# Kernel tuning notes

Measured on AMD Instinct MI355X. Metric: run time of the kernel, lower is better.

## Reference

```python
import jax, jax.numpy as jnp
import numpy as np
from functools import partial

INPUT_DIM = 256
HIDDEN = 512
NUM_LAYERS = 2

def _linp(key, fan_in, shape):
    # torch nn.Linear/Conv default init: U(-1/sqrt(fan_in), 1/sqrt(fan_in))
    bound = 1.0 / np.sqrt(fan_in)
    return jax.random.uniform(key, shape, jnp.float32, -bound, bound)

def setup_inputs() -> dict:
    key = jax.random.key(0)
    ks = iter(jax.random.split(key, 64))
    d = {}
    d["x"] = jax.random.normal(next(ks), (32, 16, 1, 64, 64), jnp.float32)
    # encoder convs (OIHW)
    d["conv1_w"] = _linp(next(ks), 1 * 9, (16, 1, 3, 3));   d["conv1_b"] = _linp(next(ks), 1 * 9, (16,))
    d["conv2_w"] = _linp(next(ks), 16 * 9, (32, 16, 3, 3)); d["conv2_b"] = _linp(next(ks), 16 * 9, (32,))
    d["conv3_w"] = _linp(next(ks), 32 * 9, (INPUT_DIM, 32, 3, 3)); d["conv3_b"] = _linp(next(ks), 32 * 9, (INPUT_DIM,))
    # LSTM cells: per layer 4 gate linears (forget, input, cell, output), in = input+hidden
    for j in range(NUM_LAYERS):
        fan = (INPUT_DIM if j == 0 else HIDDEN) + HIDDEN
        for g in ("f", "i", "g", "o"):
            d[f"W{g}{j}"] = _linp(next(ks), fan, (fan, HIDDEN))
            d[f"b{g}{j}"] = _linp(next(ks), fan, (HIDDEN,))
    # classifier
    d["cw1"] = _linp(next(ks), HIDDEN, (HIDDEN, 128)); d["cb1"] = _linp(next(ks), HIDDEN, (128,))
    d["cw2"] = _linp(next(ks), 128, (128, 64));        d["cb2"] = _linp(next(ks), 128, (64,))
    d["cw3"] = _linp(next(ks), 64, (64, 6));           d["cb3"] = _linp(next(ks), 64, (6,))
    return d

def _conv(x, w, b):
    y = jax.lax.conv_general_dilated(x, w, (1, 1), "SAME",
                                     dimension_numbers=("NCHW", "OIHW", "NCHW"))
    return y + b[None, :, None, None]

def _maxpool2(x):
    return jax.lax.reduce_window(x, -jnp.inf, jax.lax.max,
                                 (1, 1, 2, 2), (1, 1, 2, 2), "VALID")

def reference(x, conv1_w, conv1_b, conv2_w, conv2_b, conv3_w, conv3_b,
              Wf0, bf0, Wi0, bi0, Wg0, bg0, Wo0, bo0,
              Wf1, bf1, Wi1, bi1, Wg1, bg1, Wo1, bo1,
              cw1, cb1, cw2, cb2, cw3, cb3):
    B, T, C, H, W = x.shape
    xf = x.reshape(B * T, C, H, W)
    h = _maxpool2(jax.nn.relu(_conv(xf, conv1_w, conv1_b)))
    h = _maxpool2(jax.nn.relu(_conv(h, conv2_w, conv2_b)))
    h = jax.nn.relu(_conv(h, conv3_w, conv3_b))
    emb = h.mean(axis=(2, 3)).reshape(B, T, -1)  # AdaptiveAvgPool2d((1,1)); dropout = identity (eval)

    layers = [(Wf0, bf0, Wi0, bi0, Wg0, bg0, Wo0, bo0),
              (Wf1, bf1, Wi1, bi1, Wg1, bg1, Wo1, bo1)]

    def step(carry, x_t):
        hs, cs = carry
        inp = x_t
        new_h, new_c = [], []
        for j, (Wf, bf, Wi, bi, Wg, bg, Wo, bo) in enumerate(layers):
            comb = jnp.concatenate([inp, hs[j]], axis=1)  # [B, in+H]
            f_t = jax.nn.sigmoid(comb @ Wf + bf)
            i_t = jax.nn.sigmoid(comb @ Wi + bi)
            g_t = jnp.tanh(comb @ Wg + bg)
            o_t = jax.nn.sigmoid(comb @ Wo + bo)
            c_n = f_t * cs[j] + i_t * g_t
            h_n = o_t * jnp.tanh(c_n)
            new_h.append(h_n); new_c.append(c_n)
            inp = h_n
        return (tuple(new_h), tuple(new_c)), None

    h0 = tuple(jnp.zeros((B, HIDDEN), x.dtype) for _ in range(NUM_LAYERS))
    c0 = tuple(jnp.zeros((B, HIDDEN), x.dtype) for _ in range(NUM_LAYERS))
    (hs, _), _ = jax.lax.scan(step, (h0, c0), jnp.swapaxes(emb, 0, 1))
    last = hs[-1]  # [B, HIDDEN], last timestep top-layer h (dropout = identity)

    y = jax.nn.relu(last @ cw1 + cb1)
    y = jax.nn.relu(y @ cw2 + cb2)
    return y @ cw3 + cb3  # [B, 6]
```

## Files before the change

### kernel.cpp

```cpp
#include <hip/hip_runtime.h>
#include <math.h>

__global__ void k_conv1(const float* __restrict__ x, const float* __restrict__ w,
                        const float* __restrict__ bias, float* __restrict__ out) {
  int idx = blockIdx.x * 256 + threadIdx.x;
  int ox = idx & 31, oy = (idx >> 5) & 31, oc = (idx >> 10) & 15, n = idx >> 14;
  const float* im = x + n * 4096;
  float wv[9];
#pragma unroll
  for (int i = 0; i < 9; ++i) wv[i] = w[oc * 9 + i];
  float bs = bias[oc];
  float m = 0.f;
#pragma unroll
  for (int dy = 0; dy < 2; ++dy)
#pragma unroll
    for (int dx = 0; dx < 2; ++dx) {
      int cy = oy * 2 + dy, cx = ox * 2 + dx;
      float s = bs;
#pragma unroll
      for (int ky = 0; ky < 3; ++ky) {
        int yy = cy + ky - 1;
        if (yy < 0 || yy >= 64) continue;
#pragma unroll
        for (int kx = 0; kx < 3; ++kx) {
          int xx = cx + kx - 1;
          if (xx < 0 || xx >= 64) continue;
          s += im[yy * 64 + xx] * wv[ky * 3 + kx];
        }
      }
      m = fmaxf(m, fmaxf(s, 0.f));
    }
  out[idx] = m;
}

__global__ void k_prep_w(const float* __restrict__ w2, float* __restrict__ w2t,
                         const float* __restrict__ w3, float* __restrict__ w3t) {
  int id = blockIdx.x * 256 + threadIdx.x;
  if (id < 73728) {
    int ct = id >> 8, oc = id & 255;
    int c = ct / 9, tap = ct - 9 * c;
    w3t[id] = w3[(oc * 32 + c) * 9 + tap];
  }
  if (id < 4608) {
    int ct = id >> 5, oc = id & 31;
    int c = ct / 9, tap = ct - 9 * c;
    w2t[id] = w2[(oc * 16 + c) * 9 + tap];
  }
}

__global__ __launch_bounds__(256) void k_conv2(
    const float* __restrict__ a1, const float* __restrict__ w2t,
    const float* __restrict__ bias, float* __restrict__ a2) {
  __shared__ __align__(16) float ins[8 * 1024];
  int n = blockIdx.x, ocg = blockIdx.y;
  int tid = threadIdx.x;
  int py = tid >> 4, px = tid & 15;
  int y0 = 2 * py - 1, x0 = 2 * px - 1;
  float acc[16][4] = {};
  const float* wb = w2t + ocg * 16;
  for (int ph = 0; ph < 2; ++ph) {
    __syncthreads();
    const float4* src = (const float4*)(a1 + n * 16384 + ph * 8192);
    for (int i = tid; i < 2048; i += 256) ((float4*)ins)[i] = src[i];
    __syncthreads();
    for (int c = 0; c < 8; ++c) {
      float wv[4][4];
#pragma unroll
      for (int r = 0; r < 4; ++r) {
        int y = y0 + r;
        bool vy = (y >= 0) && (y < 32);
        int yc = vy ? y : 0;
#pragma unroll
        for (int cc = 0; cc < 4; ++cc) {
          int xx = x0 + cc;
          bool vx = (xx >= 0) && (xx < 32);
          int xc = vx ? xx : 0;
          float t = ins[c * 1024 + yc * 32 + xc];
          wv[r][cc] = (vy && vx) ? t : 0.f;
        }
      }
      int ch = ph * 8 + c;
#pragma unroll
      for (int ky = 0; ky < 3; ++ky)
#pragma unroll
        for (int kx = 0; kx < 3; ++kx) {
          const float* w16 = wb + (ch * 9 + ky * 3 + kx) * 32;
#pragma unroll
          for (int i = 0; i < 4; ++i) {
            float vv = wv[(i >> 1) + ky][(i & 1) + kx];
#pragma unroll
            for (int j = 0; j < 16; ++j) acc[j][i] += vv * w16[j];
          }
        }
    }
  }
  const float* bp = bias + ocg * 16;
  float4 o[4];
#pragma unroll
  for (int j = 0; j < 16; ++j) {
    float m = fmaxf(fmaxf(acc[j][0], acc[j][1]), fmaxf(acc[j][2], acc[j][3]));
    ((float*)o)[j] = fmaxf(m + bp[j], 0.f);
  }
  float4* dst = (float4*)(a2 + (size_t)(n * 256 + tid) * 32 + ocg * 16);
#pragma unroll
  for (int q = 0; q < 4; ++q) dst[q] = o[q];
}

__global__ __launch_bounds__(256) void k_conv3(
    const float* __restrict__ a2, const float* __restrict__ w3t,
    const float* __restrict__ bias, float* __restrict__ comb0) {
  __shared__ __align__(16) float ins[324 * 12];
  float4* ins4 = (float4*)ins;
  int n = blockIdx.x, ocb = blockIdx.y;
  int tid = threadIdx.x;
  for (int i = tid; i < 972; i += 256) ins4[i] = float4{0.f, 0.f, 0.f, 0.f};
  int wvid = __builtin_amdgcn_readfirstlane(tid >> 6);
  int lane = tid & 63;
  int tr = lane >> 4, tc = lane & 15;
  float acc[4][8] = {};
  const float* wbase = w3t + ocb * 32 + wvid * 8;
  const float4* src = (const float4*)(a2 + (size_t)n * 8192);
  for (int ph = 0; ph < 4; ++ph) {
    __syncthreads();
    for (int i = tid; i < 512; i += 256) {
      int px = i >> 1, cg = i & 1;
      int p = ((px >> 4) + 1) * 18 + (px & 15) + 1;
      ins4[p * 3 + cg] = src[px * 8 + ph * 2 + cg];
    }
    __syncthreads();
    for (int cg = 0; cg < 2; ++cg) {
      float4 v[6][3];
#pragma unroll
      for (int dr = 0; dr < 6; ++dr)
#pragma unroll
        for (int dc = 0; dc < 3; ++dc)
          v[dr][dc] = ins4[((4 * tr + dr) * 18 + tc + dc) * 3 + cg];
      int chb = ph * 8 + cg * 4;
#pragma unroll
      for (int ky = 0; ky < 3; ++ky)
#pragma unroll
        for (int kx = 0; kx < 3; ++kx)
#pragma unroll
          for (int c = 0; c < 4; ++c) {
            const float* w8 = wbase + ((chb + c) * 9 + ky * 3 + kx) * 256;
#pragma unroll
            for (int i = 0; i < 4; ++i) {
              float vv = ((const float*)&v[i + ky][kx])[c];
#pragma unroll
              for (int j = 0; j < 8; ++j) acc[i][j] += vv * w8[j];
            }
          }
    }
  }
  const float* bp = bias + ocb * 32 + wvid * 8;
  int bb = n >> 4, tt = n & 15;
#pragma unroll
  for (int j = 0; j < 8; ++j) {
    float bj = bp[j];
    float s = 0.f;
#pragma unroll
    for (int i = 0; i < 4; ++i) s += fmaxf(acc[i][j] + bj, 0.f);
#pragma unroll
    for (int off = 32; off; off >>= 1) s += __shfl_down(s, off, 64);
    if (lane == 0) {
      int oc = ocb * 32 + wvid * 8 + j;
      comb0[(size_t)(tt * 768 + oc) * 32 + bb] = s * (1.f / 256.f);
    }
  }
}

__global__ void k_pack(const float* __restrict__ Wf, const float* __restrict__ Wi,
                       const float* __restrict__ Wg, const float* __restrict__ Wo,
                       float* __restrict__ p, int fan) {
  __shared__ float t[4][32][33];
  int k0 = blockIdx.x * 32, h0 = blockIdx.y * 32;
  int tx = threadIdx.x & 31, ty = threadIdx.x >> 5;
  const float* Ws[4] = {Wf, Wi, Wg, Wo};
#pragma unroll
  for (int g = 0; g < 4; ++g)
    for (int r = 0; r < 32; r += 8)
      t[g][ty + r][tx] = Ws[g][(size_t)(k0 + ty + r) * 512 + h0 + tx];
  __syncthreads();
  for (int r = 0; r < 32; r += 8) {
    int hh = ty + r;
    float4 v = {t[0][tx][hh], t[1][tx][hh], t[2][tx][hh], t[3][tx][hh]};
    ((float4*)p)[(size_t)(h0 + hh) * fan + k0 + tx] = v;
  }
}

struct Coop2Args {
  float* comb0; float* comb1;
  const float* p0; const float* p1;
  const float* b00; const float* b01; const float* b02; const float* b03;
  const float* b10; const float* b11; const float* b12; const float* b13;
  int* bar;
};

#define COOP2_LDS_BYTES (32512 * 4)

#define FMA4(acc, s, a)                                   \
  acc.x += (s) * (a).x; acc.y += (s) * (a).y;             \
  acc.z += (s) * (a).z; acc.w += (s) * (a).w;

template <bool DO0, bool DO1>
__device__ __forceinline__ void fused_step(
    int hbase, int tid, int it, const Coop2Args& A,
    const float4* __restrict__ w40, const float4* __restrict__ w41,
    float* __restrict__ gsum, float* __restrict__ pre0,
    float* __restrict__ pre1,
    float bf0, float bi0, float bg0, float bo0,
    float bf1, float bi1, float bg1, float bo1,
    float& c0reg, float& c1reg) {
  const int C0 = 768 * 32, C1 = 1024 * 32;
  const int kc = tid >> 3, bq = tid & 7;
  float4 p0f{0,0,0,0}, p0i{0,0,0,0}, p0g{0,0,0,0}, p0o{0,0,0,0};
  float4 p1f{0,0,0,0}, p1i{0,0,0,0}, p1g{0,0,0,0}, p1o{0,0,0,0};
  float4 q0f{0,0,0,0}, q0i{0,0,0,0}, q0g{0,0,0,0}, q0o{0,0,0,0};
  float4 q1f{0,0,0,0}, q1i{0,0,0,0}, q1g{0,0,0,0}, q1o{0,0,0,0};
  if constexpr (DO1) {
    const float4* a41 = (const float4*)(A.comb1 + (size_t)(it - 1) * C1)
                        + kc * 8 + bq;
#pragma unroll
    for (int kk = 0; kk < 16; ++kk) {
      float4 a = a41[kk * 512];
      float4 u = w41[kk * 64];
      float4 v = w41[1024 + kk * 64];
      FMA4(q0f, u.x, a) FMA4(q0i, u.y, a) FMA4(q0g, u.z, a) FMA4(q0o, u.w, a)
      FMA4(q1f, v.x, a) FMA4(q1i, v.y, a) FMA4(q1g, v.z, a) FMA4(q1o, v.w, a)
    }
  }
  if constexpr (DO0) {
    const float4* a40 = (const float4*)(A.comb0 + (size_t)it * C0)
                        + kc * 8 + bq;
#pragma unroll
    for (int kk = 0; kk < 12; ++kk) {
      float4 a = a40[kk * 512];
      float4 u = w40[kk * 64];
      float4 v = w40[768 + kk * 64];
      FMA4(p0f, u.x, a) FMA4(p0i, u.y, a) FMA4(p0g, u.z, a) FMA4(p0o, u.w, a)
      FMA4(p1f, v.x, a) FMA4(p1i, v.y, a) FMA4(p1g, v.z, a) FMA4(p1o, v.w, a)
    }
  }
#define GW(hsv, gv, acc) {                                            \
    float* _r = gsum + (size_t)(((hsv) * 4 + (gv)) * 32 + 4 * bq) * 67 + kc; \
    _r[0] = acc.x; _r[67] = acc.y; _r[134] = acc.z; _r[201] = acc.w; }
  __syncthreads();
  if constexpr (DO0) {
    GW(0, 0, p0f) GW(0, 1, p0i) GW(0, 2, p0g) GW(0, 3, p0o)
    GW(1, 0, p1f) GW(1, 1, p1i) GW(1, 2, p1g) GW(1, 3, p1o)
  }
  __syncthreads();
  if constexpr (DO0) {
    int row = tid & 255, half = tid >> 8;
    const float* gp = gsum + (size_t)row * 67 + half * 32;
    float s = 0.f;
#pragma unroll
    for (int q = 0; q < 32; ++q) s += gp[q];
    pre0[half * 256 + row] = s;
  }
  __syncthreads();
  if constexpr (DO1) {
    GW(0, 0, q0f) GW(0, 1, q0i) GW(0, 2, q0g) GW(0, 3, q0o)
    GW(1, 0, q1f) GW(1, 1, q1i) GW(1, 2, q1g) GW(1, 3, q1o)
  }
  __syncthreads();
  if constexpr (DO1) {
    int row = tid & 255, half = tid >> 8;
    const float* gp = gsum + (size_t)row * 67 + half * 32;
    float s = 0.f;
#pragma unroll
    for (int q = 0; q < 32; ++q) s += gp[q];
    pre1[half * 256 + row] = s;
  }
  __syncthreads();
#undef GW
  if (tid < 64) {
    int hs2 = tid >> 5, b = tid & 31, hh = hbase + hs2;
    int r = hs2 * 128 + b;
    if constexpr (DO0) {
      float fp = pre0[r] + pre0[256 + r] + bf0;
      float ip = pre0[r + 32] + pre0[256 + r + 32] + bi0;
      float gp = pre0[r + 64] + pre0[256 + r + 64] + bg0;
      float op = pre0[r + 96] + pre0[256 + r + 96] + bo0;
      float ft = 1.f / (1.f + expf(-fp));
      float it_ = 1.f / (1.f + expf(-ip));
      float gt = tanhf(gp);
      float ot = 1.f / (1.f + expf(-op));
      float cn = ft * c0reg + it_ * gt;
      c0reg = cn;
      float hn = ot * tanhf(cn);
      float* hA = A.comb0 + (size_t)(it + 1) * C0 + 256 * 32;
      float* hB = A.comb1 + (size_t)it * C1;
      __hip_atomic_store(&hA[hh * 32 + b], hn, __ATOMIC_RELAXED,
                         __HIP_MEMORY_SCOPE_AGENT);
      __hip_atomic_store(&hB[hh * 32 + b], hn, __ATOMIC_RELAXED,
                         __HIP_MEMORY_SCOPE_AGENT);
    }
    if constexpr (DO1) {
      float fp = pre1[r] + pre1[256 + r] + bf1;
      float ip = pre1[r + 32] + pre1[256 + r + 32] + bi1;
      float gp = pre1[r + 64] + pre1[256 + r + 64] + bg1;
      float op = pre1[r + 96] + pre1[256 + r + 96] + bo1;
      float ft = 1.f / (1.f + expf(-fp));
      float it_ = 1.f / (1.f + expf(-ip));
      float gt = tanhf(gp);
      float ot = 1.f / (1.f + expf(-op));
      float cn = ft * c1reg + it_ * gt;
      c1reg = cn;
      float hn = ot * tanhf(cn);
      float* hA = A.comb1 + (size_t)it * C1 + 512 * 32;
      __hip_atomic_store(&hA[hh * 32 + b], hn, __ATOMIC_RELAXED,
                         __HIP_MEMORY_SCOPE_AGENT);
    }
  }
}

__device__ __forceinline__ void coop_barrier(int* bars, int tid, int bid,
                                             int it) {
  __syncthreads();
  if (tid == 0) {
    int* gb = bars + 32 + (bid & 7) * 32;
    int old = __hip_atomic_fetch_add(gb, 1, __ATOMIC_ACQ_REL,
                                     __HIP_MEMORY_SCOPE_AGENT);
    if (old == 32 * (it + 1) - 1)
      __hip_atomic_fetch_add(bars, 1, __ATOMIC_RELEASE,
                             __HIP_MEMORY_SCOPE_AGENT);
    while (__hip_atomic_load(bars, __ATOMIC_RELAXED,
                             __HIP_MEMORY_SCOPE_AGENT) < 8 * (it + 1))
      __builtin_amdgcn_s_sleep(2);
    __builtin_amdgcn_fence(__ATOMIC_ACQUIRE, "agent");
  }
  __syncthreads();
}

__global__ __launch_bounds__(512, 2) void k_lstm_coop2(Coop2Args A) {
  extern __shared__ float smem[];
  float* wl0 = smem;
  float* wl1 = smem + 6144;
  float* gsum = smem + 14336;
  float* pre0 = smem + 31488;
  float* pre1 = smem + 32000;
  const int tid = threadIdx.x;
  const int hbase = blockIdx.x * 2;
  for (int i = tid; i < 1536; i += 512) {
    int hs = (i >= 768), k = i - hs * 768;
    ((float4*)wl0)[hs * 768 + k] =
        ((const float4*)A.p0)[(size_t)(hbase + hs) * 768 + k];
  }
  for (int i = tid; i < 2048; i += 512) {
    int hs = i >> 10, k = i & 1023;
    ((float4*)wl1)[hs * 1024 + k] =
        ((const float4*)A.p1)[(size_t)(hbase + hs) * 1024 + k];
  }
  float bf0 = 0, bi0 = 0, bg0 = 0, bo0 = 0;
  float bf1 = 0, bi1 = 0, bg1 = 0, bo1 = 0;
  float c0reg = 0.f, c1reg = 0.f;
  if (tid < 64) {
    int hh = hbase + (tid >> 5);
    bf0 = A.b00[hh]; bi0 = A.b01[hh]; bg0 = A.b02[hh]; bo0 = A.b03[hh];
    bf1 = A.b10[hh]; bi1 = A.b11[hh]; bg1 = A.b12[hh]; bo1 = A.b13[hh];
  }
  __syncthreads();
  const int kc = tid >> 3;
  const float4* w40 = (const float4*)wl0 + kc;
  const float4* w41 = (const float4*)wl1 + kc;

  fused_step<true, false>(hbase, tid, 0, A, w40, w41, gsum, pre0, pre1,
                          bf0, bi0, bg0, bo0, bf1, bi1, bg1, bo1, c0reg, c1reg);
  coop_barrier(A.bar, tid, blockIdx.x, 0);
  for (int it = 1; it < 16; ++it) {
    fused_step<true, true>(hbase, tid, it, A, w40, w41, gsum, pre0, pre1,
                           bf0, bi0, bg0, bo0, bf1, bi1, bg1, bo1, c0reg, c1reg);
    coop_barrier(A.bar, tid, blockIdx.x, it);
  }
  fused_step<false, true>(hbase, tid, 16, A, w40, w41, gsum, pre0, pre1,
                          bf0, bi0, bg0, bo0, bf1, bi1, bg1, bo1, c0reg, c1reg);
}

struct SArgs {
  const float* comb; const float* pw;
  float* houtA; float* houtB; float* cT;
  const float* bf; const float* bi; const float* bg; const float* bo;
};

template <int FAN>
__device__ __forceinline__ void lstm_sbody(int h, int tid, const SArgs& A,
                                           float* __restrict__ gsum) {
  constexpr int CH = FAN / 8;
  const int wv = __builtin_amdgcn_readfirstlane(tid >> 6);
  const int lane = tid & 63;
  const int ks = lane >> 5, b = lane & 31;
  const int kb = wv * CH;
  const float4* pw4 = (const float4*)A.pw + (size_t)h * FAN + kb;
  const float* ac = A.comb + (size_t)kb * 32 + lane;
  float a0 = 0.f, a1 = 0.f, a2 = 0.f, a3 = 0.f;
#pragma unroll 8
  for (int kk = 0; kk < CH; kk += 2) {
    float4 w0 = pw4[kk];
    float4 w1 = pw4[kk + 1];
    float av = ac[kk * 32];
    a0 += av * (ks ? w1.x : w0.x);
    a1 += av * (ks ? w1.y : w0.y);
    a2 += av * (ks ? w1.z : w0.z);
    a3 += av * (ks ? w1.w : w0.w);
  }
  a0 += __shfl_xor(a0, 32);
  a1 += __shfl_xor(a1, 32);
  a2 += __shfl_xor(a2, 32);
  a3 += __shfl_xor(a3, 32);
  if (lane < 32) {
    gsum[(wv * 4 + 0) * 33 + b] = a0;
    gsum[(wv * 4 + 1) * 33 + b] = a1;
    gsum[(wv * 4 + 2) * 33 + b] = a2;
    gsum[(wv * 4 + 3) * 33 + b] = a3;
  }
  __syncthreads();
  if (tid < 32) {
    float fp = A.bf[h], ip = A.bi[h], gp = A.bg[h], op = A.bo[h];
#pragma unroll
    for (int q = 0; q < 8; ++q) {
      fp += gsum[(q * 4 + 0) * 33 + tid];
      ip += gsum[(q * 4 + 1) * 33 + tid];
      gp += gsum[(q * 4 + 2) * 33 + tid];
      op += gsum[(q * 4 + 3) * 33 + tid];
    }
    float ft = 1.f / (1.f + expf(-fp));
    float it_ = 1.f / (1.f + expf(-ip));
    float gt = tanhf(gp);
    float ot = 1.f / (1.f + expf(-op));
    float cn = ft * A.cT[h * 32 + tid] + it_ * gt;
    A.cT[h * 32 + tid] = cn;
    float hn = ot * tanhf(cn);
    A.houtA[h * 32 + tid] = hn;
    A.houtB[h * 32 + tid] = hn;
  }
}

__global__ __launch_bounds__(512) void k_lstm_s0(SArgs a) {
  __shared__ float gsum[32 * 33];
  lstm_sbody<768>(blockIdx.x, threadIdx.x, a, gsum);
}
__global__ __launch_bounds__(512) void k_lstm_s1(SArgs a) {
  __shared__ float gsum[32 * 33];
  lstm_sbody<1024>(blockIdx.x, threadIdx.x, a, gsum);
}
__global__ __launch_bounds__(512) void k_lstm_spair(SArgs a0, SArgs a1) {
  __shared__ float gsum[32 * 33];
  if (blockIdx.x < 512)
    lstm_sbody<768>(blockIdx.x, threadIdx.x, a0, gsum);
  else
    lstm_sbody<1024>(blockIdx.x - 512, threadIdx.x, a1, gsum);
}

__global__ void k_cls(const float* __restrict__ h1T, const float* __restrict__ cw1,
                      const float* __restrict__ cb1, const float* __restrict__ cw2,
                      const float* __restrict__ cb2, const float* __restrict__ cw3,
                      const float* __restrict__ cb3, float* __restrict__ out) {
  __shared__ float hv[512];
  __shared__ float y1[128];
  __shared__ float y2[64];
  int b = blockIdx.x, tid = threadIdx.x;
  for (int i = tid; i < 512; i += 128) hv[i] = h1T[i * 32 + b];
  __syncthreads();
  float s = cb1[tid];
  for (int k = 0; k < 512; ++k) s += hv[k] * cw1[k * 128 + tid];
  y1[tid] = fmaxf(s, 0.f);
  __syncthreads();
  if (tid < 64) {
    float s2 = cb2[tid];
    for (int k = 0; k < 128; ++k) s2 += y1[k] * cw2[k * 64 + tid];
    y2[tid] = fmaxf(s2, 0.f);
  }
  __syncthreads();
  if (tid < 6) {
    float s3 = cb3[tid];
    for (int k = 0; k < 64; ++k) s3 += y2[k] * cw3[k * 6 + tid];
    out[b * 6 + tid] = s3;
  }
}

extern "C" void kernel_launch(void* const* d_in, const int* in_sizes, int n_in,
                              void* d_out, int out_size, void* d_ws, size_t ws_size,
                              hipStream_t stream) {
  const float* x  = (const float*)d_in[0];
  const float* w1 = (const float*)d_in[1];
  const float* b1 = (const float*)d_in[2];
  const float* w2 = (const float*)d_in[3];
  const float* b2 = (const float*)d_in[4];
  const float* w3 = (const float*)d_in[5];
  const float* b3 = (const float*)d_in[6];
  const float* cw1 = (const float*)d_in[23];
  const float* cb1 = (const float*)d_in[24];
  const float* cw2 = (const float*)d_in[25];
  const float* cb2 = (const float*)d_in[26];
  const float* cw3 = (const float*)d_in[27];
  const float* cb3 = (const float*)d_in[28];

  float* ws = (float*)d_ws;
  float* a1    = ws;
  float* p0    = ws;
  float* p1    = ws + 1572864;
  float* comb0 = ws + 3670016;
  float* comb1 = ws + 4087808;
  float* c0    = ws + 4644864;
  float* c1    = ws + 4661248;
  int*   bar   = (int*)(ws + 4677632);
  float* a2    = ws + 8388608;
  float* w2t   = ws + 12582912;
  float* w3t   = ws + 12587520;
  const int C0 = 768 * 32, C1 = 1024 * 32;

  k_prep_w<<<288, 256, 0, stream>>>(w2, w2t, w3, w3t);
  k_conv1<<<32768, 256, 0, stream>>>(x, w1, b1, a1);
  k_conv2<<<dim3(512, 2), 256, 0, stream>>>(a1, w2t, b2, a2);

  hipMemsetAsync(comb0 + 256 * 32, 0, (size_t)512 * 32 * 4, stream);
  hipMemsetAsync(comb1 + 512 * 32, 0, (size_t)512 * 32 * 4, stream);
  hipMemsetAsync(c0, 0, (size_t)2 * 512 * 32 * 4, stream);
  hipMemsetAsync(bar, 0, 512 * sizeof(int), stream);

  k_conv3<<<dim3(512, 8), 256, 0, stream>>>(a2, w3t, b3, comb0);

  k_pack<<<dim3(24, 16), 256, 0, stream>>>(
      (const float*)d_in[7], (const float*)d_in[9],
      (const float*)d_in[11], (const float*)d_in[13], p0, 768);
  k_pack<<<dim3(32, 16), 256, 0, stream>>>(
      (const float*)d_in[15], (const float*)d_in[17],
      (const float*)d_in[19], (const float*)d_in[21], p1, 1024);

  Coop2Args ca;
  ca.comb0 = comb0; ca.comb1 = comb1;
  ca.p0 = p0; ca.p1 = p1;
  ca.b00 = (const float*)d_in[8];  ca.b01 = (const float*)d_in[10];
  ca.b02 = (const float*)d_in[12]; ca.b03 = (const float*)d_in[14];
  ca.b10 = (const float*)d_in[16]; ca.b11 = (const float*)d_in[18];
  ca.b12 = (const float*)d_in[20]; ca.b13 = (const float*)d_in[22];
  ca.bar = bar;
  void* kargs[] = {&ca};
  hipError_t cerr = hipLaunchCooperativeKernel(
      (void*)k_lstm_coop2, dim3(256), dim3(512), kargs, COOP2_LDS_BYTES, stream);

  if (cerr != hipSuccess) {
    auto L0 = [&](int t) {
      SArgs a;
      a.comb = comb0 + (size_t)t * C0;
      a.pw = p0;
      a.houtA = comb0 + (size_t)(t + 1) * C0 + 256 * 32;
      a.houtB = comb1 + (size_t)t * C1;
      a.cT = c0;
      a.bf = (const float*)d_in[8];  a.bi = (const float*)d_in[10];
      a.bg = (const float*)d_in[12]; a.bo = (const float*)d_in[14];
      return a;
    };
    auto L1 = [&](int t) {
      SArgs a;
      a.comb = comb1 + (size_t)t * C1;
      a.pw = p1;
      a.houtA = comb1 + (size_t)(t + 1) * C1 + 512 * 32;
      a.houtB = a.houtA;
      a.cT = c1;
      a.bf = (const float*)d_in[16]; a.bi = (const float*)d_in[18];
      a.bg = (const float*)d_in[20]; a.bo = (const float*)d_in[22];
      return a;
    };
    k_lstm_s0<<<512, 512, 0, stream>>>(L0(0));
    for (int p = 0; p < 15; ++p)
      k_lstm_spair<<<1024, 512, 0, stream>>>(L0(p + 1), L1(p));
    k_lstm_s1<<<512, 512, 0, stream>>>(L1(15));
  }

  k_cls<<<32, 128, 0, stream>>>(comb1 + (size_t)16 * C1 + 512 * 32,
                                cw1, cb1, cw2, cb2, cw3, cb3, (float*)d_out);
}
```

Measured before the change: 631.8 us.

## Widen conv3 per-wave output channels to 16 and stream input taps

Each wave of the conv3 kernel now computes 16 output channels instead of 8, using float4 accumulators and float4 weight loads, so the grid's channel dimension halves from 8 to 4 blocks. The inner loop is reordered to load each LDS input vector once and scatter it across the ky taps, replacing the 6x3 float4 register tile. This doubles reuse of each LDS input read and vectorises the weight loads, at the cost of more accumulator registers, possible lower occupancy, and fewer blocks.

```diff
diff --git a/kernel.cpp b/kernel.cpp
--- a/kernel.cpp
+++ b/kernel.cpp
@@ -106,6 +106,10 @@
   for (int q = 0; q < 4; ++q) dst[q] = o[q];
 }
 
+#define FMA4(acc, s, a)                                   \
+  acc.x += (s) * (a).x; acc.y += (s) * (a).y;             \
+  acc.z += (s) * (a).z; acc.w += (s) * (a).w;
+
 __global__ __launch_bounds__(256) void k_conv3(
     const float* __restrict__ a2, const float* __restrict__ w3t,
     const float* __restrict__ bias, float* __restrict__ comb0) {
@@ -117,9 +121,14 @@
   int wvid = __builtin_amdgcn_readfirstlane(tid >> 6);
   int lane = tid & 63;
   int tr = lane >> 4, tc = lane & 15;
-  float acc[4][8] = {};
-  const float* wbase = w3t + ocb * 32 + wvid * 8;
+  float4 a00{0,0,0,0}, a01{0,0,0,0}, a02{0,0,0,0}, a03{0,0,0,0};
+  float4 a10{0,0,0,0}, a11{0,0,0,0}, a12{0,0,0,0}, a13{0,0,0,0};
+  float4 a20{0,0,0,0}, a21{0,0,0,0}, a22{0,0,0,0}, a23{0,0,0,0};
+  float4 a30{0,0,0,0}, a31{0,0,0,0}, a32{0,0,0,0}, a33{0,0,0,0};
+  const float* wbase = w3t + ocb * 64 + wvid * 16;
   const float4* src = (const float4*)(a2 + (size_t)n * 8192);
+#define TAPROW(A0, A1, A2, A3) \
+  { FMA4(A0, vv, w0) FMA4(A1, vv, w1) FMA4(A2, vv, w2) FMA4(A3, vv, w3) }
   for (int ph = 0; ph < 4; ++ph) {
     __syncthreads();
     for (int i = tid; i < 512; i += 256) {
@@ -129,44 +138,56 @@
     }
     __syncthreads();
     for (int cg = 0; cg < 2; ++cg) {
-      float4 v[6][3];
-#pragma unroll
-      for (int dr = 0; dr < 6; ++dr)
-#pragma unroll
-        for (int dc = 0; dc < 3; ++dc)
-          v[dr][dc] = ins4[((4 * tr + dr) * 18 + tc + dc) * 3 + cg];
       int chb = ph * 8 + cg * 4;
 #pragma unroll
-      for (int ky = 0; ky < 3; ++ky)
-#pragma unroll
-        for (int kx = 0; kx < 3; ++kx)
+      for (int dr = 0; dr < 6; ++dr) {
+#pragma unroll
+        for (int dc = 0; dc < 3; ++dc) {
+          float4 v = ins4[((4 * tr + dr) * 18 + tc + dc) * 3 + cg];
 #pragma unroll
           for (int c = 0; c < 4; ++c) {
-            const float* w8 = wbase + ((chb + c) * 9 + ky * 3 + kx) * 256;
-#pragma unroll
-            for (int i = 0; i < 4; ++i) {
-              float vv = ((const float*)&v[i + ky][kx])[c];
-#pragma unroll
-              for (int j = 0; j < 8; ++j) acc[i][j] += vv * w8[j];
+            float vv = ((const float*)&v)[c];
+#pragma unroll
+            for (int ky = 0; ky < 3; ++ky) {
+              int i2 = dr - ky;
+              if (i2 >= 0 && i2 < 4) {
+                const float4* w4 =
+                    (const float4*)(wbase + ((chb + c) * 9 + ky * 3 + dc) * 256);
+                float4 w0 = w4[0], w1 = w4[1], w2 = w4[2], w3 = w4[3];
+                if (i2 == 0) TAPROW(a00, a01, a02, a03)
+                else if (i2 == 1) TAPROW(a10, a11, a12, a13)
+                else if (i2 == 2) TAPROW(a20, a21, a22, a23)
+                else TAPROW(a30, a31, a32, a33)
+              }
             }
           }
-    }
-  }
-  const float* bp = bias + ocb * 32 + wvid * 8;
+        }
+      }
+    }
+  }
+#undef TAPROW
+  const float* bp = bias + ocb * 64 + wvid * 16;
   int bb = n >> 4, tt = n & 15;
-#pragma unroll
-  for (int j = 0; j < 8; ++j) {
-    float bj = bp[j];
-    float s = 0.f;
-#pragma unroll
-    for (int i = 0; i < 4; ++i) s += fmaxf(acc[i][j] + bj, 0.f);
-#pragma unroll
-    for (int off = 32; off; off >>= 1) s += __shfl_down(s, off, 64);
-    if (lane == 0) {
-      int oc = ocb * 32 + wvid * 8 + j;
-      comb0[(size_t)(tt * 768 + oc) * 32 + bb] = s * (1.f / 256.f);
-    }
-  }
+#define EPI(Q, A0, A1, A2, A3)                                          \
+  _Pragma("unroll")                                                     \
+  for (int e = 0; e < 4; ++e) {                                         \
+    float bj = bp[(Q) * 4 + e];                                         \
+    float s = fmaxf(((const float*)&(A0))[e] + bj, 0.f);                \
+    s += fmaxf(((const float*)&(A1))[e] + bj, 0.f);                     \
+    s += fmaxf(((const float*)&(A2))[e] + bj, 0.f);                     \
+    s += fmaxf(((const float*)&(A3))[e] + bj, 0.f);                     \
+    _Pragma("unroll")                                                   \
+    for (int off = 32; off; off >>= 1) s += __shfl_down(s, off, 64);    \
+    if (lane == 0) {                                                    \
+      int oc = ocb * 64 + wvid * 16 + (Q) * 4 + e;                      \
+      comb0[(size_t)(tt * 768 + oc) * 32 + bb] = s * (1.f / 256.f);     \
+    }                                                                   \
+  }
+  EPI(0, a00, a10, a20, a30)
+  EPI(1, a01, a11, a21, a31)
+  EPI(2, a02, a12, a22, a32)
+  EPI(3, a03, a13, a23, a33)
+#undef EPI
 }
 
 __global__ void k_pack(const float* __restrict__ Wf, const float* __restrict__ Wi,
@@ -197,10 +218,6 @@
 };
 
 #define COOP2_LDS_BYTES (32512 * 4)
-
-#define FMA4(acc, s, a)                                   \
-  acc.x += (s) * (a).x; acc.y += (s) * (a).y;             \
-  acc.z += (s) * (a).z; acc.w += (s) * (a).w;
 
 template <bool DO0, bool DO1>
 __device__ __forceinline__ void fused_step(
@@ -519,7 +536,7 @@
   hipMemsetAsync(c0, 0, (size_t)2 * 512 * 32 * 4, stream);
   hipMemsetAsync(bar, 0, 512 * sizeof(int), stream);
 
-  k_conv3<<<dim3(512, 8), 256, 0, stream>>>(a2, w3t, b3, comb0);
+  k_conv3<<<dim3(512, 4), 256, 0, stream>>>(a2, w3t, b3, comb0);
 
   k_pack<<<dim3(24, 16), 256, 0, stream>>>(
       (const float*)d_in[7], (const float*)d_in[9],
```

Result: slower. 1.355 ms (+114.5%).
